# Performance work log

Measured on AMD Instinct MI355X. Metric: run time of the kernel, lower is better.

Reference implementation:

```python
import jax, jax.numpy as jnp
import numpy as np

N_NODES = 80000
N_EDGES = 800000
N_REL = 400
D_IN = 256
D_OUT = 256
BN_EPS = 1e-5


def _xavier(key, shape, gain=np.sqrt(2.0)):
    fan_in, fan_out = shape[0], shape[-1]
    std = gain * np.sqrt(2.0 / (fan_in + fan_out))
    return jax.random.normal(key, shape, dtype=jnp.float32) * std


def ccorr(a, b):
    # circular correlation: irfft(conj(rfft(a)) * rfft(b), n)
    n = a.shape[-1]
    return jnp.fft.irfft(jnp.conj(jnp.fft.rfft(a)) * jnp.fft.rfft(b), n)


def setup_inputs() -> dict:
    key = jax.random.key(0)
    ks = jax.random.split(key, 12)
    x = jax.random.normal(ks[0], (N_NODES, D_IN), dtype=jnp.float32)
    rel_repr = jax.random.normal(ks[1], (N_REL, D_IN), dtype=jnp.float32)
    edge_src = jax.random.randint(ks[2], (N_EDGES,), 0, N_NODES)
    edge_dst = jax.random.randint(ks[3], (N_EDGES,), 0, N_NODES)
    edge_type = jax.random.randint(ks[4], (N_EDGES,), 0, N_REL)
    edge_norm = jax.random.uniform(ks[5], (N_EDGES,), dtype=jnp.float32)
    in_w = _xavier(ks[6], (D_IN, D_OUT))
    out_w = _xavier(ks[7], (D_IN, D_OUT))
    loop_w = _xavier(ks[8], (D_IN, D_OUT))
    w_rel = _xavier(ks[9], (D_IN, D_OUT))
    loop_rel = _xavier(ks[10], (1, D_IN))
    bias = jnp.zeros((D_OUT,), dtype=jnp.float32)
    return {"x": x, "rel_repr": rel_repr, "edge_src": edge_src,
            "edge_dst": edge_dst, "edge_type": edge_type, "edge_norm": edge_norm,
            "in_w": in_w, "out_w": out_w, "loop_w": loop_w, "w_rel": w_rel,
            "loop_rel": loop_rel, "bias": bias}


def reference(x, rel_repr, edge_src, edge_dst, edge_type, edge_norm,
              in_w, out_w, loop_w, w_rel, loop_rel, bias):
    E = edge_src.shape[0]
    half = E // 2
    # gather + compose (opn == 'corr')
    h_src = x[edge_src]                         # [E, D_in]
    edge_data = ccorr(h_src, rel_repr[edge_type])  # [E, D_in]
    # direction-split matmul
    msg = jnp.concatenate([edge_data[:half] @ in_w,
                           edge_data[half:] @ out_w], axis=0)  # [E, D_out]
    msg = msg * edge_norm[:, None]
    # scatter-sum into destination nodes, then reduce (dropout p=0, /3)
    agg = jax.ops.segment_sum(msg, edge_dst, num_segments=x.shape[0]) / 3.0
    # self-loop
    loop = ccorr(x, jnp.broadcast_to(loop_rel, x.shape)) @ loop_w / 3.0
    out = agg + loop + bias
    # BatchNorm1d (training mode: batch stats, gamma=1, beta=0)
    mean = jnp.mean(out, axis=0)
    var = jnp.var(out, axis=0)
    out = (out - mean) / jnp.sqrt(var + BN_EPS)
    # act is identity
    return out, rel_repr @ w_rel
```

## Files before the change

kernel.cpp:

```cpp
#include <hip/hip_runtime.h>

#define NN 80000
#define NE 800000
#define EH 400000
#define NR 400
#define DD 256
#define FD 256
#define KP 768
#define NB 160000
#define NCH 157
#define MT 80400
#define PI2 6.283185307179586f

typedef unsigned short u16;
typedef __attribute__((ext_vector_type(8))) short bf16x8;
typedef __attribute__((ext_vector_type(4))) float f32x4;

static __device__ __forceinline__ float bu2f(u16 u) {
  return __uint_as_float(((unsigned int)u) << 16);
}
static __device__ __forceinline__ u16 f2bu(float f) {
  unsigned int x = __float_as_uint(f);
  x += 0x7fffu + ((x >> 16) & 1u);
  return (u16)(x >> 16);
}
static __device__ __forceinline__ unsigned int pk2(float a, float b) {
  return (unsigned int)f2bu(a) | ((unsigned int)f2bu(b) << 16);
}
static __device__ __forceinline__ void gload16(const void* g, void* l) {
  __builtin_amdgcn_global_load_lds(
      (const __attribute__((address_space(1))) unsigned int*)g,
      (__attribute__((address_space(3))) unsigned int*)l, 16, 0, 0);
}

__global__ void k_build(const float* __restrict__ in_w, const float* __restrict__ out_w,
                        const float* __restrict__ lr, const float* __restrict__ loop_w,
                        u16* __restrict__ Ft, u16* __restrict__ Bt) {
  __shared__ float L[DD];
  int bb = blockIdx.x, c = threadIdx.x;
  if (bb < 256) {
    int row = bb, j = c;
    int k, im;
    if (row == 0)      { k = 0;   im = 0; }
    else if (row == 1) { k = 128; im = 0; }
    else               { k = row >> 1; im = row & 1; }
    int m = (j * k) & 255;
    float th = -PI2 * (float)m * (1.0f / 256.0f);
    Ft[row * 256 + j] = f2bu(im ? sinf(th) : cosf(th));
  } else if (bb < 768) {
    int t = bb - 256;
    const float* W = (t < 256) ? in_w : out_w;
    int tp = t & 255;
    int k, im; float alpha;
    if (tp == 0)      { k = 0;   im = 0; alpha = 1.0f; }
    else if (tp == 1) { k = 128; im = 0; alpha = 1.0f; }
    else              { k = tp >> 1; im = tp & 1; alpha = 2.0f; }
    float scale = alpha * (1.0f / 768.0f);
    int m = (c * k) & 255;
    float th = -PI2 * (float)m * (1.0f / 256.0f);
    L[c] = im ? sinf(th) : cosf(th);
    __syncthreads();
    float acc = 0.0f;
    for (int j = 0; j < DD; ++j)
      acc += L[j] * W[(size_t)j * DD + c];
    Bt[(size_t)c * KP + t] = f2bu(scale * acc);
  } else {
    int j = bb - 768;
    L[c] = lr[c];
    __syncthreads();
    float acc = 0.0f;
    for (int k2 = 0; k2 < DD; ++k2)
      acc += L[(j + k2) & 255] * loop_w[(size_t)k2 * DD + c];
    Bt[(size_t)c * KP + 512 + j] = f2bu(acc * (1.0f / 3.0f));
  }
}

__global__ __launch_bounds__(512) void k_dft(
    const float* __restrict__ x, const float* __restrict__ rel,
    const u16* __restrict__ Ft, u16* __restrict__ xfh, u16* __restrict__ rfh,
    u16* __restrict__ Ap) {
  __shared__ u16 sA[2][128 * 64];
  __shared__ u16 sB[256 * 64];
  int tid = threadIdx.x;
  int w = tid >> 6, lane = tid & 63;
  int r0 = blockIdx.x * 128;
  int wm = (w & 1) * 64, wn = (w >> 1) * 64;
  int fr = lane & 15, fg = lane >> 4;

  int arow = tid >> 2;
  int acg = (tid & 3) * 16;
  int gr = r0 + arow;
  int grc = gr < MT ? gr : MT - 1;
  const float* asrc = (grc < NN) ? (x + (size_t)grc * DD)
                                 : (rel + (size_t)(grc - NN) * DD);
  bool doAp = (gr < NN);

  float4 a0_, a1_, a2_, a3_;
#define LOADA(kb) { const float* p_ = asrc + (kb) * 64 + acg;                     \
    a0_ = *(const float4*)(p_);     a1_ = *(const float4*)(p_ + 4);               \
    a2_ = *(const float4*)(p_ + 8); a3_ = *(const float4*)(p_ + 12); }

#define STGB(kb) { _Pragma("unroll") for (int q = 0; q < 4; ++q) {                \
    int s_ = w * 4 + q; int c_ = 8 * s_ + (lane >> 3);                            \
    int cb_ = (lane & 7) ^ (c_ & 7);                                              \
    gload16(Ft + (size_t)c_ * 256 + (kb) * 64 + cb_ * 8, sB + s_ * 512); } }

#define CVTA(kb, buf) {                                                           \
    uint4 c0_ = make_uint4(pk2(a0_.x, a0_.y), pk2(a0_.z, a0_.w),                  \
                           pk2(a1_.x, a1_.y), pk2(a1_.z, a1_.w));                 \
    uint4 c1_ = make_uint4(pk2(a2_.x, a2_.y), pk2(a2_.z, a2_.w),                  \
                           pk2(a3_.x, a3_.y), pk2(a3_.z, a3_.w));                 \
    int b0_ = (tid & 3) * 2;                                                      \
    *(uint4*)(sA[buf] + arow * 64 + ((b0_ ^ (arow & 7)) * 8)) = c0_;              \
    *(uint4*)(sA[buf] + arow * 64 + (((b0_ + 1) ^ (arow & 7)) * 8)) = c1_;        \
    if (doAp) { u16* ap_ = Ap + (size_t)gr * KP + 512 + (kb) * 64 + acg;          \
      *(uint4*)(ap_) = c0_; *(uint4*)(ap_ + 8) = c1_; } }

  f32x4 acc[4][4];
#pragma unroll
  for (int i = 0; i < 4; ++i)
#pragma unroll
    for (int j = 0; j < 4; ++j) acc[i][j] = (f32x4){0.f, 0.f, 0.f, 0.f};

  LOADA(0)
  STGB(0)
  CVTA(0, 0)
  LOADA(1)
  __syncthreads();
  for (int kb = 0; kb < 4; ++kb) {
    int cur = kb & 1;
#pragma unroll
    for (int ks = 0; ks < 2; ++ks) {
      bf16x8 af[4], bfr[4];
#pragma unroll
      for (int mt = 0; mt < 4; ++mt) {
        int r = wm + mt * 16 + fr;
        af[mt] = *(const bf16x8*)(sA[cur] + r * 64 + ((ks * 32 + fg * 8) ^ ((r & 7) * 8)));
      }
#pragma unroll
      for (int nt = 0; nt < 4; ++nt) {
        int c = wn + nt * 16 + fr;
        bfr[nt] = *(const bf16x8*)(sB + c * 64 + ((ks * 32 + fg * 8) ^ ((c & 7) * 8)));
      }
#pragma unroll
      for (int mt = 0; mt < 4; ++mt)
#pragma unroll
        for (int nt = 0; nt < 4; ++nt)
          acc[mt][nt] = __builtin_amdgcn_mfma_f32_16x16x32_bf16(af[mt], bfr[nt],
                                                                acc[mt][nt], 0, 0, 0);
    }
    __syncthreads();
    if (kb < 3) {
      STGB(kb + 1)
      CVTA(kb + 1, cur ^ 1)
      if (kb < 2) LOADA(kb + 2)
      __syncthreads();
    }
  }
#undef LOADA
#undef STGB
#undef CVTA

#pragma unroll
  for (int mt = 0; mt < 4; ++mt)
#pragma unroll
    for (int nt = 0; nt < 4; ++nt) {
      int cg = wn + nt * 16 + fr;
#pragma unroll
      for (int j = 0; j < 4; ++j) {
        int rg = r0 + wm + mt * 16 + fg * 4 + j;
        u16 val = f2bu(acc[mt][nt][j]);
        if (rg < NN)      xfh[(size_t)rg * FD + cg] = val;
        else if (rg < MT) rfh[(size_t)(rg - NN) * FD + cg] = val;
      }
    }
}

__global__ void k_hist(const int* __restrict__ edst, int* __restrict__ cnt) {
  int e = blockIdx.x * 256 + threadIdx.x;
  int key = edst[e] + ((e >= EH) ? NN : 0);
  atomicAdd(&cnt[key], 1);
}

__global__ __launch_bounds__(256) void k_scan1(const int* __restrict__ cnt,
                                               int* __restrict__ base,
                                               int* __restrict__ chunkTot) {
  __shared__ int wsum[4];
  int t = threadIdx.x;
  int g0 = blockIdx.x * 1024 + t * 4;
  int v[4], ex[4], s = 0;
#pragma unroll
  for (int j = 0; j < 4; ++j) v[j] = (g0 + j < NB) ? cnt[g0 + j] : 0;
#pragma unroll
  for (int j = 0; j < 4; ++j) { ex[j] = s; s += v[j]; }
  int lane = t & 63, w = t >> 6;
  int inc = s;
  for (int off = 1; off < 64; off <<= 1) {
    int n = __shfl_up(inc, off);
    if (lane >= off) inc += n;
  }
  if (lane == 63) wsum[w] = inc;
  __syncthreads();
  int woff = 0;
  for (int i = 0; i < w; ++i) woff += wsum[i];
  int exth = woff + inc - s;
#pragma unroll
  for (int j = 0; j < 4; ++j)
    if (g0 + j < NB) base[g0 + j] = exth + ex[j];
  if (t == 255) chunkTot[blockIdx.x] = woff + inc;
}

__global__ __launch_bounds__(256) void k_scan2(const int* __restrict__ chunkTot,
                                               int* __restrict__ chunkOff) {
  __shared__ int wsum[4];
  int t = threadIdx.x;
  int v = (t < NCH) ? chunkTot[t] : 0;
  int lane = t & 63, w = t >> 6;
  int inc = v;
  for (int off = 1; off < 64; off <<= 1) {
    int n = __shfl_up(inc, off);
    if (lane >= off) inc += n;
  }
  if (lane == 63) wsum[w] = inc;
  __syncthreads();
  int woff = 0;
  for (int i = 0; i < w; ++i) woff += wsum[i];
  if (t < NCH) chunkOff[t] = woff + inc - v;
}

__global__ void k_scan3(int* __restrict__ base, const int* __restrict__ chunkOff,
                        int* __restrict__ cursor) {
  int i = blockIdx.x * 256 + threadIdx.x;
  if (i < NB) {
    int b = base[i] + chunkOff[i >> 10];
    base[i] = b;
    cursor[i] = b;
  }
  if (i == 0) base[NB] = NE;
}

__global__ void k_scatter(const int* __restrict__ esrc, const int* __restrict__ edst,
                          const int* __restrict__ etyp, const float* __restrict__ enorm,
                          int* __restrict__ cursor, int4* __restrict__ recs) {
  int e = blockIdx.x * 256 + threadIdx.x;
  int key = edst[e] + ((e >= EH) ? NN : 0);
  int pos = atomicAdd(&cursor[key], 1);
  recs[pos] = make_int4(esrc[e], etyp[e], __float_as_int(enorm[e]), 0);
}

__global__ __launch_bounds__(256) void k_reduce(
    const u16* __restrict__ xfh, const u16* __restrict__ rfh,
    const int4* __restrict__ recs, const int* __restrict__ base,
    u16* __restrict__ Ap) {
  int w = threadIdx.x >> 6, lane = threadIdx.x & 63;
  int b = blockIdx.x * 4 + w;
  int start = base[b], end = base[b + 1];
  bool l0 = (lane == 0);
  float a0 = 0, a1 = 0, a2 = 0, a3 = 0;
  int p = start;
  for (; p + 3 < end; p += 4) {
    ushort4 xv[4], rv[4];
    float nm[4];
#pragma unroll
    for (int u = 0; u < 4; ++u) {
      int4 rc = recs[p + u];
      nm[u] = __int_as_float(rc.z);
      xv[u] = *(const ushort4*)(xfh + (size_t)rc.x * FD + 4 * lane);
      rv[u] = *(const ushort4*)(rfh + (size_t)rc.y * FD + 4 * lane);
    }
#pragma unroll
    for (int u = 0; u < 4; ++u) {
      float xr0 = bu2f(xv[u].x), xi0 = bu2f(xv[u].y);
      float xr1 = bu2f(xv[u].z), xi1 = bu2f(xv[u].w);
      float rr0 = bu2f(rv[u].x), ri0 = bu2f(rv[u].y);
      float rr1 = bu2f(rv[u].z), ri1 = bu2f(rv[u].w);
      float p0 = l0 ? (xr0 * rr0) : (xr0 * rr0 + xi0 * ri0);
      float p1 = l0 ? (xi0 * ri0) : (xr0 * ri0 - xi0 * rr0);
      a0 += p0 * nm[u];
      a1 += p1 * nm[u];
      a2 += (xr1 * rr1 + xi1 * ri1) * nm[u];
      a3 += (xr1 * ri1 - xi1 * rr1) * nm[u];
    }
  }
  for (; p < end; ++p) {
    int4 rc = recs[p];
    float nm0 = __int_as_float(rc.z);
    ushort4 xv0 = *(const ushort4*)(xfh + (size_t)rc.x * FD + 4 * lane);
    ushort4 rv0 = *(const ushort4*)(rfh + (size_t)rc.y * FD + 4 * lane);
    float xr0 = bu2f(xv0.x), xi0 = bu2f(xv0.y), xr1 = bu2f(xv0.z), xi1 = bu2f(xv0.w);
    float rr0 = bu2f(rv0.x), ri0 = bu2f(rv0.y), rr1 = bu2f(rv0.z), ri1 = bu2f(rv0.w);
    float p0 = l0 ? (xr0 * rr0) : (xr0 * rr0 + xi0 * ri0);
    float p1 = l0 ? (xi0 * ri0) : (xr0 * ri0 - xi0 * rr0);
    a0 += p0 * nm0;
    a1 += p1 * nm0;
    a2 += (xr1 * rr1 + xi1 * ri1) * nm0;
    a3 += (xr1 * ri1 - xi1 * rr1) * nm0;
  }
  u16* tp = Ap + ((b < NN) ? (size_t)b * KP : (size_t)(b - NN) * KP + 256);
  *(unsigned int*)(tp + 4 * lane)     = pk2(a0, a1);
  *(unsigned int*)(tp + 4 * lane + 2) = pk2(a2, a3);
}

__global__ __launch_bounds__(512) void k_mgemm(
    const u16* __restrict__ Ap, const u16* __restrict__ Bt,
    const float* __restrict__ bias, u16* __restrict__ doutb,
    float* __restrict__ sum1, float* __restrict__ sum2) {
  __shared__ u16 sA[2][128 * 64];
  __shared__ u16 sB[256 * 64];
  int tid = threadIdx.x;
  int w = tid >> 6, lane = tid & 63;
  int r0 = blockIdx.x * 128;
  int wm = (w & 1) * 64, wn = (w >> 1) * 64;
  int fr = lane & 15, fg = lane >> 4;

#define STGA(kb, buf) { _Pragma("unroll") for (int q = 0; q < 2; ++q) {           \
    int s_ = w * 2 + q; int r_ = 8 * s_ + (lane >> 3);                            \
    int cb_ = (lane & 7) ^ (r_ & 7);                                              \
    gload16(Ap + (size_t)(r0 + r_) * KP + (kb) * 64 + cb_ * 8,                    \
            sA[buf] + s_ * 512); } }

#define STGB(kb) { _Pragma("unroll") for (int q = 0; q < 4; ++q) {                \
    int s_ = w * 4 + q; int c_ = 8 * s_ + (lane >> 3);                            \
    int cb_ = (lane & 7) ^ (c_ & 7);                                              \
    gload16(Bt + (size_t)c_ * KP + (kb) * 64 + cb_ * 8, sB + s_ * 512); } }

  f32x4 acc[4][4];
#pragma unroll
  for (int i = 0; i < 4; ++i)
#pragma unroll
    for (int j = 0; j < 4; ++j) acc[i][j] = (f32x4){0.f, 0.f, 0.f, 0.f};

  STGA(0, 0)
  STGB(0)
  __syncthreads();
  for (int kb = 0; kb < 12; ++kb) {
    int cur = kb & 1;
    if (kb < 11) STGA(kb + 1, cur ^ 1)
#pragma unroll
    for (int ks = 0; ks < 2; ++ks) {
      bf16x8 af[4], bfr[4];
#pragma unroll
      for (int mt = 0; mt < 4; ++mt) {
        int r = wm + mt * 16 + fr;
        af[mt] = *(const bf16x8*)(sA[cur] + r * 64 + ((ks * 32 + fg * 8) ^ ((r & 7) * 8)));
      }
#pragma unroll
      for (int nt = 0; nt < 4; ++nt) {
        int c = wn + nt * 16 + fr;
        bfr[nt] = *(const bf16x8*)(sB + c * 64 + ((ks * 32 + fg * 8) ^ ((c & 7) * 8)));
      }
#pragma unroll
      for (int mt = 0; mt < 4; ++mt)
#pragma unroll
        for (int nt = 0; nt < 4; ++nt)
          acc[mt][nt] = __builtin_amdgcn_mfma_f32_16x16x32_bf16(af[mt], bfr[nt],
                                                                acc[mt][nt], 0, 0, 0);
    }
    __syncthreads();
    if (kb < 11) { STGB(kb + 1) __syncthreads(); }
  }
#undef STGA
#undef STGB

  float s1[4] = {0.f, 0.f, 0.f, 0.f}, s2[4] = {0.f, 0.f, 0.f, 0.f};
#pragma unroll
  for (int nt = 0; nt < 4; ++nt) {
    int cg = wn + nt * 16 + fr;
    float bv = bias[cg];
#pragma unroll
    for (int mt = 0; mt < 4; ++mt) {
#pragma unroll
      for (int j = 0; j < 4; ++j) {
        int rg = r0 + wm + mt * 16 + fg * 4 + j;
        float val = acc[mt][nt][j] + bv;
        doutb[(size_t)rg * DD + cg] = f2bu(val);
        s1[nt] += val;
        s2[nt] += val * val;
      }
    }
  }
#pragma unroll
  for (int nt = 0; nt < 4; ++nt) {
    s1[nt] += __shfl_xor(s1[nt], 16); s1[nt] += __shfl_xor(s1[nt], 32);
    s2[nt] += __shfl_xor(s2[nt], 16); s2[nt] += __shfl_xor(s2[nt], 32);
  }
  if (lane < 16) {
#pragma unroll
    for (int nt = 0; nt < 4; ++nt) {
      atomicAdd(&sum1[wn + nt * 16 + lane], s1[nt]);
      atomicAdd(&sum2[wn + nt * 16 + lane], s2[nt]);
    }
  }
}

__global__ __launch_bounds__(256) void k_norm(const u16* __restrict__ doutb,
                                              float* __restrict__ out,
                                              const float* __restrict__ sum1,
                                              const float* __restrict__ sum2) {
  size_t tid0 = (size_t)blockIdx.x * 256 + threadIdx.x;
  int c0 = (int)((tid0 * 4) & 255);
  float m[4], rs[4];
#pragma unroll
  for (int j = 0; j < 4; ++j) {
    float mm = sum1[c0 + j] * (1.0f / (float)NN);
    float var = sum2[c0 + j] * (1.0f / (float)NN) - mm * mm;
    m[j] = mm;
    rs[j] = rsqrtf(var + 1e-5f);
  }
  size_t total = (size_t)NN * DD / 4;
  size_t stride = (size_t)gridDim.x * 256;
  for (size_t i = tid0; i < total; i += stride) {
    uint2 q = *((const uint2*)doutb + i);
    float4 v;
    v.x = (bu2f((u16)q.x) - m[0]) * rs[0];
    v.y = (bu2f((u16)(q.x >> 16)) - m[1]) * rs[1];
    v.z = (bu2f((u16)q.y) - m[2]) * rs[2];
    v.w = (bu2f((u16)(q.y >> 16)) - m[3]) * rs[3];
    *((float4*)out + i) = v;
  }
}

__global__ void k_rel(const float* __restrict__ rel, const float* __restrict__ wrel,
                      float* __restrict__ out2) {
  __shared__ float R[DD];
  int r = blockIdx.x, c = threadIdx.x;
  R[c] = rel[(size_t)r * DD + c];
  __syncthreads();
  float acc = 0.0f;
  for (int j = 0; j < DD; ++j)
    acc += R[j] * wrel[(size_t)j * DD + c];
  out2[(size_t)r * DD + c] = acc;
}

__global__ void k_fail(float* __restrict__ out, int n) {
  int i = blockIdx.x * 256 + threadIdx.x;
  if (i < n) out[i] = 1.0e6f;
}

extern "C" void kernel_launch(void* const* d_in, const int* in_sizes, int n_in,
                              void* d_out, int out_size, void* d_ws, size_t ws_size,
                              hipStream_t stream) {
  (void)in_sizes; (void)n_in;
  const float* x      = (const float*)d_in[0];
  const float* rel    = (const float*)d_in[1];
  const int*   esrc   = (const int*)d_in[2];
  const int*   edst   = (const int*)d_in[3];
  const int*   etyp   = (const int*)d_in[4];
  const float* enorm  = (const float*)d_in[5];
  const float* in_w   = (const float*)d_in[6];
  const float* out_w  = (const float*)d_in[7];
  const float* loop_w = (const float*)d_in[8];
  const float* w_rel  = (const float*)d_in[9];
  const float* lr     = (const float*)d_in[10];
  const float* bias   = (const float*)d_in[11];
  float* dout = (float*)d_out;

  char* wsb = (char*)d_ws;
  size_t off = 0;
  u16* Apack = (u16*)(wsb + off); off += (size_t)NN * KP * 2;
  u16* Bt    = (u16*)(wsb + off); off += (size_t)DD * KP * 2;
  u16* xfh   = (u16*)(wsb + off); off += (size_t)NN * FD * 2;
  u16* rfh   = (u16*)(wsb + off); off += (size_t)NR * FD * 2;
  u16* Ft    = (u16*)(wsb + off); off += (size_t)DD * DD * 2;
  u16* doutb = (u16*)(wsb + off); off += (size_t)NN * DD * 2;
  int4* recs = (int4*)(wsb + off); off += (size_t)NE * 16;
  float* sum1  = (float*)(wsb + off); off += DD * 4;
  float* sum2  = (float*)(wsb + off); off += DD * 4;
  int* cnt   = (int*)(wsb + off); off += (size_t)(NB + 1) * 4;
  int* baseA = (int*)(wsb + off); off += (size_t)(NB + 1) * 4;
  int* curA  = (int*)(wsb + off); off += (size_t)NB * 4;
  int* chT   = (int*)(wsb + off); off += 256 * 4;
  int* chO   = (int*)(wsb + off); off += 256 * 4;

  if (ws_size < off) {
    k_fail<<<(out_size + 255) / 256, 256, 0, stream>>>(dout, out_size);
    return;
  }

  hipMemsetAsync(cnt, 0, (NB + 1) * sizeof(int), stream);
  hipMemsetAsync(sum1, 0, 2 * DD * sizeof(float), stream);
  k_build<<<1024, 256, 0, stream>>>(in_w, out_w, lr, loop_w, Ft, Bt);
  k_hist<<<NE / 256, 256, 0, stream>>>(edst, cnt);
  k_scan1<<<NCH, 256, 0, stream>>>(cnt, baseA, chT);
  k_scan2<<<1, 256, 0, stream>>>(chT, chO);
  k_scan3<<<(NB + 255) / 256, 256, 0, stream>>>(baseA, chO, curA);
  k_scatter<<<NE / 256, 256, 0, stream>>>(esrc, edst, etyp, enorm, curA, recs);
  k_dft<<<(MT + 127) / 128, 512, 0, stream>>>(x, rel, Ft, xfh, rfh, Apack);
  k_reduce<<<NB / 4, 256, 0, stream>>>(xfh, rfh, recs, baseA, Apack);
  k_mgemm<<<NN / 128, 512, 0, stream>>>(Apack, Bt, bias, doutb, sum1, sum2);
  k_norm<<<2048, 256, 0, stream>>>(doutb, dout, sum1, sum2);
  k_rel<<<NR, 256, 0, stream>>>(rel, w_rel, dout + (size_t)NN * DD);
}
```

Before: 371.2 us.

## Pack edge records to 8 bytes, merge small kernels and memsets, use packed math

```diff
diff --git a/kernel.cpp b/kernel.cpp
--- a/kernel.cpp
+++ b/kernel.cpp
@@ -15,6 +15,7 @@
 typedef unsigned short u16;
 typedef __attribute__((ext_vector_type(8))) short bf16x8;
 typedef __attribute__((ext_vector_type(4))) float f32x4;
+typedef __attribute__((ext_vector_type(2))) float f32x2;
 
 static __device__ __forceinline__ float bu2f(u16 u) {
   return __uint_as_float(((unsigned int)u) << 16);
@@ -35,9 +36,16 @@
 
 __global__ void k_build(const float* __restrict__ in_w, const float* __restrict__ out_w,
                         const float* __restrict__ lr, const float* __restrict__ loop_w,
+                        const int* __restrict__ edst, int* __restrict__ cnt,
                         u16* __restrict__ Ft, u16* __restrict__ Bt) {
   __shared__ float L[DD];
   int bb = blockIdx.x, c = threadIdx.x;
+  if (bb >= 1024) {
+    int e = (bb - 1024) * 256 + c;
+    int key = edst[e] + ((e >= EH) ? NN : 0);
+    atomicAdd(&cnt[key], 1);
+    return;
+  }
   if (bb < 256) {
     int row = bb, j = c;
     int k, im;
@@ -176,12 +184,6 @@
     }
 }
 
-__global__ void k_hist(const int* __restrict__ edst, int* __restrict__ cnt) {
-  int e = blockIdx.x * 256 + threadIdx.x;
-  int key = edst[e] + ((e >= EH) ? NN : 0);
-  atomicAdd(&cnt[key], 1);
-}
-
 __global__ __launch_bounds__(256) void k_scan1(const int* __restrict__ cnt,
                                                int* __restrict__ base,
                                                int* __restrict__ chunkTot) {
@@ -241,32 +243,34 @@
 
 __global__ void k_scatter(const int* __restrict__ esrc, const int* __restrict__ edst,
                           const int* __restrict__ etyp, const float* __restrict__ enorm,
-                          int* __restrict__ cursor, int4* __restrict__ recs) {
+                          int* __restrict__ cursor, uint2* __restrict__ recs) {
   int e = blockIdx.x * 256 + threadIdx.x;
   int key = edst[e] + ((e >= EH) ? NN : 0);
   int pos = atomicAdd(&cursor[key], 1);
-  recs[pos] = make_int4(esrc[e], etyp[e], __float_as_int(enorm[e]), 0);
+  recs[pos] = make_uint2((unsigned int)esrc[e] | ((unsigned int)etyp[e] << 17),
+                         __float_as_uint(enorm[e]));
 }
 
 __global__ __launch_bounds__(256) void k_reduce(
     const u16* __restrict__ xfh, const u16* __restrict__ rfh,
-    const int4* __restrict__ recs, const int* __restrict__ base,
+    const uint2* __restrict__ recs, const int* __restrict__ base,
     u16* __restrict__ Ap) {
   int w = threadIdx.x >> 6, lane = threadIdx.x & 63;
   int b = blockIdx.x * 4 + w;
   int start = base[b], end = base[b + 1];
   bool l0 = (lane == 0);
-  float a0 = 0, a1 = 0, a2 = 0, a3 = 0;
+  f32x2 a01 = (f32x2){0.f, 0.f}, a23 = (f32x2){0.f, 0.f};
   int p = start;
   for (; p + 3 < end; p += 4) {
     ushort4 xv[4], rv[4];
     float nm[4];
 #pragma unroll
     for (int u = 0; u < 4; ++u) {
-      int4 rc = recs[p + u];
-      nm[u] = __int_as_float(rc.z);
-      xv[u] = *(const ushort4*)(xfh + (size_t)rc.x * FD + 4 * lane);
-      rv[u] = *(const ushort4*)(rfh + (size_t)rc.y * FD + 4 * lane);
+      uint2 rc = recs[p + u];
+      nm[u] = __uint_as_float(rc.y);
+      unsigned int s = rc.x & 0x1FFFFu, r = rc.x >> 17;
+      xv[u] = *(const ushort4*)(xfh + (size_t)s * FD + 4 * lane);
+      rv[u] = *(const ushort4*)(rfh + (size_t)r * FD + 4 * lane);
     }
 #pragma unroll
     for (int u = 0; u < 4; ++u) {
@@ -274,31 +278,36 @@
       float xr1 = bu2f(xv[u].z), xi1 = bu2f(xv[u].w);
       float rr0 = bu2f(rv[u].x), ri0 = bu2f(rv[u].y);
       float rr1 = bu2f(rv[u].z), ri1 = bu2f(rv[u].w);
-      float p0 = l0 ? (xr0 * rr0) : (xr0 * rr0 + xi0 * ri0);
-      float p1 = l0 ? (xi0 * ri0) : (xr0 * ri0 - xi0 * rr0);
-      a0 += p0 * nm[u];
-      a1 += p1 * nm[u];
-      a2 += (xr1 * rr1 + xi1 * ri1) * nm[u];
-      a3 += (xr1 * ri1 - xi1 * rr1) * nm[u];
+      f32x2 tc = (f32x2){xr0, xr0} * (f32x2){rr0, ri0}
+               + (f32x2){xi0, -xi0} * (f32x2){ri0, rr0};
+      f32x2 te = (f32x2){xr0, xi0} * (f32x2){rr0, ri0};
+      f32x2 t0 = l0 ? te : tc;
+      a01 += t0 * nm[u];
+      f32x2 t1 = (f32x2){xr1, xr1} * (f32x2){rr1, ri1}
+               + (f32x2){xi1, -xi1} * (f32x2){ri1, rr1};
+      a23 += t1 * nm[u];
     }
   }
   for (; p < end; ++p) {
-    int4 rc = recs[p];
-    float nm0 = __int_as_float(rc.z);
-    ushort4 xv0 = *(const ushort4*)(xfh + (size_t)rc.x * FD + 4 * lane);
-    ushort4 rv0 = *(const ushort4*)(rfh + (size_t)rc.y * FD + 4 * lane);
+    uint2 rc = recs[p];
+    float nm0 = __uint_as_float(rc.y);
+    unsigned int s = rc.x & 0x1FFFFu, r = rc.x >> 17;
+    ushort4 xv0 = *(const ushort4*)(xfh + (size_t)s * FD + 4 * lane);
+    ushort4 rv0 = *(const ushort4*)(rfh + (size_t)r * FD + 4 * lane);
     float xr0 = bu2f(xv0.x), xi0 = bu2f(xv0.y), xr1 = bu2f(xv0.z), xi1 = bu2f(xv0.w);
     float rr0 = bu2f(rv0.x), ri0 = bu2f(rv0.y), rr1 = bu2f(rv0.z), ri1 = bu2f(rv0.w);
-    float p0 = l0 ? (xr0 * rr0) : (xr0 * rr0 + xi0 * ri0);
-    float p1 = l0 ? (xi0 * ri0) : (xr0 * ri0 - xi0 * rr0);
-    a0 += p0 * nm0;
-    a1 += p1 * nm0;
-    a2 += (xr1 * rr1 + xi1 * ri1) * nm0;
-    a3 += (xr1 * ri1 - xi1 * rr1) * nm0;
+    f32x2 tc = (f32x2){xr0, xr0} * (f32x2){rr0, ri0}
+             + (f32x2){xi0, -xi0} * (f32x2){ri0, rr0};
+    f32x2 te = (f32x2){xr0, xi0} * (f32x2){rr0, ri0};
+    f32x2 t0 = l0 ? te : tc;
+    a01 += t0 * nm0;
+    f32x2 t1 = (f32x2){xr1, xr1} * (f32x2){rr1, ri1}
+             + (f32x2){xi1, -xi1} * (f32x2){ri1, rr1};
+    a23 += t1 * nm0;
   }
   u16* tp = Ap + ((b < NN) ? (size_t)b * KP : (size_t)(b - NN) * KP + 256);
-  *(unsigned int*)(tp + 4 * lane)     = pk2(a0, a1);
-  *(unsigned int*)(tp + 4 * lane + 2) = pk2(a2, a3);
+  *(unsigned int*)(tp + 4 * lane)     = pk2(a01.x, a01.y);
+  *(unsigned int*)(tp + 4 * lane + 2) = pk2(a23.x, a23.y);
 }
 
 __global__ __launch_bounds__(512) void k_mgemm(
@@ -396,8 +405,23 @@
 __global__ __launch_bounds__(256) void k_norm(const u16* __restrict__ doutb,
                                               float* __restrict__ out,
                                               const float* __restrict__ sum1,
-                                              const float* __restrict__ sum2) {
-  size_t tid0 = (size_t)blockIdx.x * 256 + threadIdx.x;
+                                              const float* __restrict__ sum2,
+                                              const float* __restrict__ rel,
+                                              const float* __restrict__ wrel,
+                                              float* __restrict__ out2) {
+  __shared__ float R[DD];
+  int bb = blockIdx.x;
+  if (bb >= 2048) {
+    int r = bb - 2048, c = threadIdx.x;
+    R[c] = rel[(size_t)r * DD + c];
+    __syncthreads();
+    float acc = 0.0f;
+    for (int j = 0; j < DD; ++j)
+      acc += R[j] * wrel[(size_t)j * DD + c];
+    out2[(size_t)r * DD + c] = acc;
+    return;
+  }
+  size_t tid0 = (size_t)bb * 256 + threadIdx.x;
   int c0 = (int)((tid0 * 4) & 255);
   float m[4], rs[4];
 #pragma unroll
@@ -408,7 +432,7 @@
     rs[j] = rsqrtf(var + 1e-5f);
   }
   size_t total = (size_t)NN * DD / 4;
-  size_t stride = (size_t)gridDim.x * 256;
+  size_t stride = (size_t)2048 * 256;
   for (size_t i = tid0; i < total; i += stride) {
     uint2 q = *((const uint2*)doutb + i);
     float4 v;
@@ -418,18 +442,6 @@
     v.w = (bu2f((u16)(q.y >> 16)) - m[3]) * rs[3];
     *((float4*)out + i) = v;
   }
-}
-
-__global__ void k_rel(const float* __restrict__ rel, const float* __restrict__ wrel,
-                      float* __restrict__ out2) {
-  __shared__ float R[DD];
-  int r = blockIdx.x, c = threadIdx.x;
-  R[c] = rel[(size_t)r * DD + c];
-  __syncthreads();
-  float acc = 0.0f;
-  for (int j = 0; j < DD; ++j)
-    acc += R[j] * wrel[(size_t)j * DD + c];
-  out2[(size_t)r * DD + c] = acc;
 }
 
 __global__ void k_fail(float* __restrict__ out, int n) {
@@ -463,7 +475,7 @@
   u16* rfh   = (u16*)(wsb + off); off += (size_t)NR * FD * 2;
   u16* Ft    = (u16*)(wsb + off); off += (size_t)DD * DD * 2;
   u16* doutb = (u16*)(wsb + off); off += (size_t)NN * DD * 2;
-  int4* recs = (int4*)(wsb + off); off += (size_t)NE * 16;
+  uint2* recs = (uint2*)(wsb + off); off += (size_t)NE * 8;
   float* sum1  = (float*)(wsb + off); off += DD * 4;
   float* sum2  = (float*)(wsb + off); off += DD * 4;
   int* cnt   = (int*)(wsb + off); off += (size_t)(NB + 1) * 4;
@@ -477,10 +489,9 @@
     return;
   }
 
-  hipMemsetAsync(cnt, 0, (NB + 1) * sizeof(int), stream);
-  hipMemsetAsync(sum1, 0, 2 * DD * sizeof(float), stream);
-  k_build<<<1024, 256, 0, stream>>>(in_w, out_w, lr, loop_w, Ft, Bt);
-  k_hist<<<NE / 256, 256, 0, stream>>>(edst, cnt);
+  hipMemsetAsync(sum1, 0, (2 * DD + NB + 1) * sizeof(int), stream);
+  k_build<<<1024 + NE / 256, 256, 0, stream>>>(in_w, out_w, lr, loop_w, edst, cnt,
+                                               Ft, Bt);
   k_scan1<<<NCH, 256, 0, stream>>>(cnt, baseA, chT);
   k_scan2<<<1, 256, 0, stream>>>(chT, chO);
   k_scan3<<<(NB + 255) / 256, 256, 0, stream>>>(baseA, chO, curA);
@@ -488,6 +499,6 @@
   k_dft<<<(MT + 127) / 128, 512, 0, stream>>>(x, rel, Ft, xfh, rfh, Apack);
   k_reduce<<<NB / 4, 256, 0, stream>>>(xfh, rfh, recs, baseA, Apack);
   k_mgemm<<<NN / 128, 512, 0, stream>>>(Apack, Bt, bias, doutb, sum1, sum2);
-  k_norm<<<2048, 256, 0, stream>>>(doutb, dout, sum1, sum2);
-  k_rel<<<NR, 256, 0, stream>>>(rel, w_rel, dout + (size_t)NN * DD);
-}
+  k_norm<<<2048 + NR, 256, 0, stream>>>(doutb, dout, sum1, sum2, rel, w_rel,
+                                        dout + (size_t)NN * DD);
+}
```

Result: faster. 356.3 us (median of 2 runs) (-4.0%).
